# Optimization experiments

Measured on AMD Instinct MI355X. Metric: run time of the kernel, lower is better.

The kernel has to match this reference:

```python
import jax, jax.numpy as jnp
import numpy as np

B, C, H, W = 4, 128, 100, 256
M = 2

def setup_inputs() -> dict:
    key = jax.random.key(0)
    ks = jax.random.split(key, 5)
    feat0 = jax.random.normal(ks[0], (B, C, H, W), jnp.float32)
    feat1 = jax.random.normal(ks[1], (B, C, H, W), jnp.float32)
    adapter_weight = jax.random.normal(ks[2], (M, C), jnp.float32)
    # conv: 1x1 Conv2d(M*C -> C); store as [C_out, C_in]
    conv_w = jax.random.normal(ks[3], (C, M * C), jnp.float32) * (1.0 / np.sqrt(M * C))
    conv_b = jnp.zeros((C,), jnp.float32)
    mlp_w = jax.random.normal(ks[4], (C, C), jnp.float32) * (1.0 / np.sqrt(C))
    mlp_b = jnp.zeros((C,), jnp.float32)
    return {"feat0": feat0, "feat1": feat1, "adapter_weight": adapter_weight,
            "conv_w": conv_w, "conv_b": conv_b, "mlp_w": mlp_w, "mlp_b": mlp_b}

def reference(feat0, feat1, adapter_weight, conv_w, conv_b, mlp_w, mlp_b):
    feats = jnp.stack([feat0, feat1], axis=0)              # [M, B, C, H, W]
    b, c, h, w = feat0.shape
    # per-modality scalar-per-channel scale, then concat on channel dim
    scaled = feats * adapter_weight[:, None, :, None, None]
    cat = scaled.transpose(1, 0, 2, 3, 4).reshape(b, -1, h, w)  # [B, M*C, H, W]
    # 1x1 conv == channel matmul
    fused = jnp.einsum('bkhw,ck->bchw', cat, conv_w) + conv_b[None, :, None, None]
    f = fused.transpose(2, 3, 0, 1).reshape(h * w, b, c)   # [(HW), B, C]
    fm = feats.transpose(0, 3, 4, 1, 2).reshape(len(feats), h * w, b, c)  # [M, (HW), B, C]
    # per-location cross-agent attention, summed over modalities
    scores = jnp.einsum('msbc,sdc->msbd', fm, f) / np.sqrt(c).astype(jnp.float32)
    attn = jax.nn.softmax(scores, axis=-1)                 # [M, (HW), B, B]
    retrieved = jnp.einsum('msbd,sdc->sbc', attn, f)       # summed over m
    out = f + jax.nn.relu(retrieved @ mlp_w.T + mlp_b)
    return out.reshape(h, w, b, c).transpose(2, 3, 0, 1)   # [B, C, H, W]
```

## Files before the change

kernel.cpp:

```cpp
#include <hip/hip_runtime.h>

#define HW 25600
#define TS 16
#define NT 1600
#define NB 256

typedef float  f32x4   __attribute__((ext_vector_type(4)));
typedef short  short8  __attribute__((ext_vector_type(8)));
typedef short  short4v __attribute__((ext_vector_type(4)));
typedef unsigned int uint2v __attribute__((ext_vector_type(2)));
typedef unsigned int uint4v __attribute__((ext_vector_type(4)));

__device__ __forceinline__ float bf2f(short h) {
    return __builtin_bit_cast(float, (unsigned)((unsigned short)h) << 16);
}
__device__ __forceinline__ unsigned cvt_pk(float a, float b) {
    unsigned r;
    asm("v_cvt_pk_bf16_f32 %0, %1, %2" : "=v"(r) : "v"(a), "v"(b));
    return r;
}

typedef __attribute__((address_space(3))) const char lds_cchar;
typedef __attribute__((address_space(3))) char lds_char;
typedef __attribute__((address_space(1))) const void g_cvoid;
__device__ __forceinline__ unsigned lds_u32(const void* p) {
    return (unsigned)(uintptr_t)(lds_cchar*)p;
}
__device__ __forceinline__ void dma16(const float* g, unsigned lds_byte) {
    __builtin_amdgcn_global_load_lds(
        (g_cvoid*)g,
        (__attribute__((address_space(3))) void*)(lds_char*)(uintptr_t)lds_byte,
        16, 0, 0);
}

__device__ __forceinline__ short4v tr_read(unsigned a) {
    short4v d;
    asm volatile("ds_read_b64_tr_b16 %0, %1" : "=v"(d) : "v"(a) : "memory");
    return d;
}
__device__ __forceinline__ short4v tr_read128(unsigned a) {
    short4v d;
    asm volatile("ds_read_b64_tr_b16 %0, %1 offset:128" : "=v"(d) : "v"(a) : "memory");
    return d;
}
__device__ __forceinline__ uint4v lds_b128(unsigned a) {
    uint4v d;
    asm volatile("ds_read_b128 %0, %1" : "=v"(d) : "v"(a) : "memory");
    return d;
}
__device__ __forceinline__ void wait_lgkm8() {
    asm volatile("s_waitcnt lgkmcnt(8)" ::: "memory");
    __builtin_amdgcn_sched_barrier(0);
}
__device__ __forceinline__ void wait_lgkm6() {
    asm volatile("s_waitcnt lgkmcnt(6)" ::: "memory");
    __builtin_amdgcn_sched_barrier(0);
}
__device__ __forceinline__ void wait_lgkm0() {
    asm volatile("s_waitcnt lgkmcnt(0)" ::: "memory");
    __builtin_amdgcn_sched_barrier(0);
}
__device__ __forceinline__ void wait_vm0() {
    asm volatile("s_waitcnt vmcnt(0)" ::: "memory");
    __builtin_amdgcn_sched_barrier(0);
}
__device__ __forceinline__ void bar_lgkm() {
    asm volatile("s_waitcnt lgkmcnt(0)" ::: "memory");
    __builtin_amdgcn_s_barrier();
    asm volatile("" ::: "memory");
}

struct Clu { short4v lo0, hi0, lo1, hi1, lo2, hi2, lo3, hi3; };
__device__ __forceinline__ void issue_clu(Clu& C, unsigned base, int tstride) {
    C.lo0 = tr_read(base);                C.hi0 = tr_read128(base);
    C.lo1 = tr_read(base + tstride);      C.hi1 = tr_read128(base + tstride);
    C.lo2 = tr_read(base + 2 * tstride);  C.hi2 = tr_read128(base + 2 * tstride);
    C.lo3 = tr_read(base + 3 * tstride);  C.hi3 = tr_read128(base + 3 * tstride);
}
__device__ __forceinline__ short8 mk8(short4v lo, short4v hi) {
    return __builtin_shufflevector(lo, hi, 0, 1, 2, 3, 4, 5, 6, 7);
}

__global__ __launch_bounds__(512, 2) void mmf_kernel(
    const float* __restrict__ feat0, const float* __restrict__ feat1,
    const float* __restrict__ adapter, const float* __restrict__ conv_w,
    const float* __restrict__ conv_b, const float* __restrict__ mlp_w,
    const float* __restrict__ mlp_b, float* __restrict__ out)
{
    __shared__ __align__(128) char smem[133120];
    float* Xf32 = (float*)smem;
    short* Xbf  = (short*)(smem + 65536);
    short* fbf  = (short*)(smem + 98304);
    short* Rbf  = (short*)(smem + 114688);
    float* sc   = (float*)(smem + 131072);

    const int tid = threadIdx.x;
    const int bid = blockIdx.x;
    const int xcd  = bid & 7;
    const int jb   = bid >> 3;
    const int tbeg = 200 * xcd + jb;
    const int tend = 200 * (xcd + 1);
    const int w   = __builtin_amdgcn_readfirstlane(tid >> 6);
    const int l   = tid & 63;
    const int g   = l >> 4;
    const int sl  = l & 15;
    const int c0  = w * 16;

    const unsigned xfbase = lds_u32(Xf32);
    const unsigned xbase  = lds_u32(Xbf);

    auto stage_dma = [&](int S) {
        #pragma unroll
        for (int i = 0; i < 8; ++i) {
            int idx = i * 512 + tid;
            int q  = idx & 3;
            int r  = idx >> 2;
            int cc = r & 127;
            int b  = (r >> 7) & 3;
            int m  = r >> 9;
            const float* fp = m ? feat1 : feat0;
            dma16(fp + (size_t)((b * 128 + cc) * HW + S + q * 4),
                  xfbase + (unsigned)((i * 512 + (w << 6)) << 4));
        }
    };

    stage_dma(tbeg * TS);

    short8 afc[8];
    #pragma unroll
    for (int ks = 0; ks < 8; ++ks) {
        const int k0 = ks * 32 + g * 8;
        const float4 w0 = *reinterpret_cast<const float4*>(conv_w + (c0 + sl) * 256 + k0);
        const float4 w1 = *reinterpret_cast<const float4*>(conv_w + (c0 + sl) * 256 + k0 + 4);
        const float4 a0 = *reinterpret_cast<const float4*>(adapter + k0);
        const float4 a1 = *reinterpret_cast<const float4*>(adapter + k0 + 4);
        uint4v au;
        au[0] = cvt_pk(w0.x * a0.x, w0.y * a0.y);
        au[1] = cvt_pk(w0.z * a0.z, w0.w * a0.w);
        au[2] = cvt_pk(w1.x * a1.x, w1.y * a1.y);
        au[3] = cvt_pk(w1.z * a1.z, w1.w * a1.w);
        afc[ks] = __builtin_bit_cast(short8, au);
    }
    short8 afm[4];
    #pragma unroll
    for (int ks = 0; ks < 4; ++ks) {
        const int k0 = ks * 32 + g * 8;
        const float4 w0 = *reinterpret_cast<const float4*>(mlp_w + (c0 + sl) * 128 + k0);
        const float4 w1 = *reinterpret_cast<const float4*>(mlp_w + (c0 + sl) * 128 + k0 + 4);
        uint4v au;
        au[0] = cvt_pk(w0.x, w0.y);
        au[1] = cvt_pk(w0.z, w0.w);
        au[2] = cvt_pk(w1.x, w1.y);
        au[3] = cvt_pk(w1.z, w1.w);
        afm[ks] = __builtin_bit_cast(short8, au);
    }
    float bias[4], mb[4];
    #pragma unroll
    for (int i = 0; i < 4; ++i) {
        bias[i] = conv_b[c0 + g * 4 + i];
        mb[i]   = mlp_b[c0 + g * 4 + i];
    }
    wait_vm0();
    bar_lgkm();

    for (int ti = tbeg; ti < tend; ti += 32) {
        const int S = ti * TS;

        #pragma unroll
        for (int i = 0; i < 8; ++i) {
            int idx = i * 512 + tid;
            const float4 v = *reinterpret_cast<const float4*>(Xf32 + (size_t)idx * 4);
            int q  = idx & 3;
            int r  = idx >> 2;
            int cc = r & 127;
            int b  = (r >> 7) & 3;
            int m  = r >> 9;
            uint2v xv;
            xv[0] = cvt_pk(v.x, v.y);
            xv[1] = cvt_pk(v.z, v.w);
            *reinterpret_cast<uint2v*>(Xbf + b * 4096 + (m * 128 + cc) * 16 + q * 4) = xv;
        }
        bar_lgkm();

        if (ti + 32 < tend) stage_dma((ti + 32) * TS);

        {
            f32x4 acc[4] = {{0,0,0,0},{0,0,0,0},{0,0,0,0},{0,0,0,0}};
            Clu cA, cB;
            issue_clu(cA, xbase + 0 * 1024 + g * 256 + sl * 8, 8192);
            #pragma unroll
            for (int ks = 0; ks < 8; ++ks) {
                Clu& cur = (ks & 1) ? cB : cA;
                Clu& nxt = (ks & 1) ? cA : cB;
                if (ks < 7) {
                    issue_clu(nxt, xbase + (ks + 1) * 1024 + g * 256 + sl * 8, 8192);
                    wait_lgkm8();
                } else {
                    wait_lgkm0();
                }
                acc[0] = __builtin_amdgcn_mfma_f32_16x16x32_bf16(afc[ks], mk8(cur.lo0, cur.hi0), acc[0], 0, 0, 0);
                acc[1] = __builtin_amdgcn_mfma_f32_16x16x32_bf16(afc[ks], mk8(cur.lo1, cur.hi1), acc[1], 0, 0, 0);
                acc[2] = __builtin_amdgcn_mfma_f32_16x16x32_bf16(afc[ks], mk8(cur.lo2, cur.hi2), acc[2], 0, 0, 0);
                acc[3] = __builtin_amdgcn_mfma_f32_16x16x32_bf16(afc[ks], mk8(cur.lo3, cur.hi3), acc[3], 0, 0, 0);
            }
            #pragma unroll
            for (int tt = 0; tt < 4; ++tt) {
                const int col = tt * 16 + sl;
                uint2v fu;
                fu[0] = cvt_pk(acc[tt][0] + bias[0], acc[tt][1] + bias[1]);
                fu[1] = cvt_pk(acc[tt][2] + bias[2], acc[tt][3] + bias[3]);
                *reinterpret_cast<uint2v*>(fbf + col * 128 + (((c0 + g * 4) ^ (sl << 3)) ^ (tt << 5))) = fu;
            }
        }
        bar_lgkm();

        {
            const int sm_m = w >> 2;
            const int sm_b = w & 3;
            const int ad = sl >> 2;
            const int aq = sl & 3;
            const unsigned fbase = lds_u32(fbf);
            const unsigned btile = xbase + sm_b * 8192 + sm_m * 4096 + g * 256 + sl * 8;
            f32x4 accS[4] = {{0,0,0,0},{0,0,0,0},{0,0,0,0},{0,0,0,0}};
            struct SC { short4v blo, bhi; uint4v a0, a1, a2, a3; };
            SC pA, pB;
            auto issue = [&](SC& Sv, int kk) {
                const unsigned bt = btile + (unsigned)(kk * 1024);
                Sv.blo = tr_read(bt); Sv.bhi = tr_read128(bt);
                const int cg = kk * 4 + g;
                Sv.a0 = lds_b128(fbase + (unsigned)((ad * 16 + 0 + aq) * 256 + (((cg ^ (0 + aq)) ^ (ad << 2)) << 4)));
                Sv.a1 = lds_b128(fbase + (unsigned)((ad * 16 + 4 + aq) * 256 + (((cg ^ (4 + aq)) ^ (ad << 2)) << 4)));
                Sv.a2 = lds_b128(fbase + (unsigned)((ad * 16 + 8 + aq) * 256 + (((cg ^ (8 + aq)) ^ (ad << 2)) << 4)));
                Sv.a3 = lds_b128(fbase + (unsigned)((ad * 16 + 12 + aq) * 256 + (((cg ^ (12 + aq)) ^ (ad << 2)) << 4)));
            };
            issue(pA, 0);
            #pragma unroll
            for (int kk = 0; kk < 4; ++kk) {
                SC& cur = (kk & 1) ? pB : pA;
                SC& nxt = (kk & 1) ? pA : pB;
                if (kk < 3) {
                    issue(nxt, kk + 1);
                    wait_lgkm6();
                } else {
                    wait_lgkm0();
                }
                const short8 bf = mk8(cur.blo, cur.bhi);
                accS[0] = __builtin_amdgcn_mfma_f32_16x16x32_bf16(__builtin_bit_cast(short8, cur.a0), bf, accS[0], 0, 0, 0);
                accS[1] = __builtin_amdgcn_mfma_f32_16x16x32_bf16(__builtin_bit_cast(short8, cur.a1), bf, accS[1], 0, 0, 0);
                accS[2] = __builtin_amdgcn_mfma_f32_16x16x32_bf16(__builtin_bit_cast(short8, cur.a2), bf, accS[2], 0, 0, 0);
                accS[3] = __builtin_amdgcn_mfma_f32_16x16x32_bf16(__builtin_bit_cast(short8, cur.a3), bf, accS[3], 0, 0, 0);
            }
            const int cstar = sl >> 2, qstar = sl & 3;
            float x = accS[0][0];
            #pragma unroll
            for (int c = 0; c < 4; ++c)
                #pragma unroll
                for (int q = 0; q < 4; ++q)
                    if (c == cstar && q == qstar) x = accS[c][q];
            x *= 0.088388347648318447f;
            float mx = fmaxf(x, __shfl_xor(x, 16));
            mx = fmaxf(mx, __shfl_xor(mx, 32));
            float e = __expf(x - mx);
            float sm = e + __shfl_xor(e, 16);
            sm += __shfl_xor(sm, 32);
            sc[(sm_m * 16 + sm_b * 4 + g) * 16 + sl] = e / sm;
        }
        bar_lgkm();

        {
            const int b = l >> 4, s = l & 15;
            float aw[4];
            #pragma unroll
            for (int d = 0; d < 4; ++d)
                aw[d] = sc[(b * 4 + d) * 16 + s] + sc[(16 + b * 4 + d) * 16 + s];
            #pragma unroll
            for (int h = 0; h < 2; ++h) {
                const int cb = w * 2 + h;
                float r[8] = {0,0,0,0,0,0,0,0};
                #pragma unroll
                for (int d = 0; d < 4; ++d) {
                    const int colf = d * 16 + s;
                    short8 fv = *reinterpret_cast<const short8*>(
                        fbf + colf * 128 + (((cb ^ s) ^ (d << 2)) << 3));
                    #pragma unroll
                    for (int e = 0; e < 8; ++e) r[e] += aw[d] * bf2f(fv[e]);
                }
                #pragma unroll
                for (int e = 0; e < 8; e += 2) {
                    unsigned uu = cvt_pk(r[e], r[e + 1]);
                    Rbf[b * 2048 + (cb * 8 + e) * 16 + s]     = (short)(uu & 0xffffu);
                    Rbf[b * 2048 + (cb * 8 + e + 1) * 16 + s] = (short)(uu >> 16);
                }
            }
        }
        bar_lgkm();

        {
            f32x4 acc[4] = {{0,0,0,0},{0,0,0,0},{0,0,0,0},{0,0,0,0}};
            const unsigned rbase = lds_u32(Rbf);
            Clu cA, cB;
            issue_clu(cA, rbase + 0 * 1024 + g * 256 + sl * 8, 4096);
            #pragma unroll
            for (int ks = 0; ks < 4; ++ks) {
                Clu& cur = (ks & 1) ? cB : cA;
                Clu& nxt = (ks & 1) ? cA : cB;
                if (ks < 3) {
                    issue_clu(nxt, rbase + (ks + 1) * 1024 + g * 256 + sl * 8, 4096);
                    wait_lgkm8();
                } else {
                    wait_lgkm0();
                }
                acc[0] = __builtin_amdgcn_mfma_f32_16x16x32_bf16(afm[ks], mk8(cur.lo0, cur.hi0), acc[0], 0, 0, 0);
                acc[1] = __builtin_amdgcn_mfma_f32_16x16x32_bf16(afm[ks], mk8(cur.lo1, cur.hi1), acc[1], 0, 0, 0);
                acc[2] = __builtin_amdgcn_mfma_f32_16x16x32_bf16(afm[ks], mk8(cur.lo2, cur.hi2), acc[2], 0, 0, 0);
                acc[3] = __builtin_amdgcn_mfma_f32_16x16x32_bf16(afm[ks], mk8(cur.lo3, cur.hi3), acc[3], 0, 0, 0);
            }
            wait_vm0();
            #pragma unroll
            for (int tt = 0; tt < 4; ++tt) {
                const int col = tt * 16 + sl;
                const short4v res = *reinterpret_cast<const short4v*>(
                    fbf + col * 128 + (((c0 + g * 4) ^ (sl << 3)) ^ (tt << 5)));
                #pragma unroll
                for (int i = 0; i < 4; ++i) {
                    const int c = c0 + g * 4 + i;
                    float v = fmaxf(acc[tt][i] + mb[i], 0.f) + bf2f(res[i]);
                    out[(size_t)(tt * 128 + c) * HW + S + sl] = v;
                }
            }
        }
        bar_lgkm();
    }
}

extern "C" void kernel_launch(void* const* d_in, const int* in_sizes, int n_in,
                              void* d_out, int out_size, void* d_ws, size_t ws_size,
                              hipStream_t stream) {
    const float* feat0   = (const float*)d_in[0];
    const float* feat1   = (const float*)d_in[1];
    const float* adapter = (const float*)d_in[2];
    const float* conv_w  = (const float*)d_in[3];
    const float* conv_b  = (const float*)d_in[4];
    const float* mlp_w   = (const float*)d_in[5];
    const float* mlp_b   = (const float*)d_in[6];
    float* out = (float*)d_out;

    dim3 grid(NB);
    dim3 block(512);
    hipLaunchKernelGGL(mmf_kernel, grid, block, 0, stream,
                       feat0, feat1, adapter, conv_w, conv_b, mlp_w, mlp_b, out);
}
```

Baseline: 49.09 us.

## Tile both GEMMs as 2x2 channel-by-batch blocks per wave to halve LDS B-fragment reads

Each wave now computes a 32-channel by 2-batch tile instead of 16 channels by all 4 batches, for both the conv GEMM and the MLP GEMM. Each B fragment read from LDS is reused across two A fragments, so per-wave transposed LDS reads drop by half, and the wait count is lowered to match the smaller prefetch. In exchange each wave holds twice as many weight fragments in registers (afc2/afm2), which raises VGPR pressure and could hurt occupancy under the 512x2 launch bounds.

After: 67.28 us. 1.37x slower.

```diff
diff --git a/kernel.cpp b/kernel.cpp
--- a/kernel.cpp
+++ b/kernel.cpp
@@ -48,8 +48,8 @@
     asm volatile("ds_read_b128 %0, %1" : "=v"(d) : "v"(a) : "memory");
     return d;
 }
-__device__ __forceinline__ void wait_lgkm8() {
-    asm volatile("s_waitcnt lgkmcnt(8)" ::: "memory");
+__device__ __forceinline__ void wait_lgkm4() {
+    asm volatile("s_waitcnt lgkmcnt(4)" ::: "memory");
     __builtin_amdgcn_sched_barrier(0);
 }
 __device__ __forceinline__ void wait_lgkm6() {
@@ -70,12 +70,10 @@
     asm volatile("" ::: "memory");
 }
 
-struct Clu { short4v lo0, hi0, lo1, hi1, lo2, hi2, lo3, hi3; };
-__device__ __forceinline__ void issue_clu(Clu& C, unsigned base, int tstride) {
+struct Clu2 { short4v lo0, hi0, lo1, hi1; };
+__device__ __forceinline__ void issue_clu2(Clu2& C, unsigned base, int tstride) {
     C.lo0 = tr_read(base);                C.hi0 = tr_read128(base);
     C.lo1 = tr_read(base + tstride);      C.hi1 = tr_read128(base + tstride);
-    C.lo2 = tr_read(base + 2 * tstride);  C.hi2 = tr_read128(base + 2 * tstride);
-    C.lo3 = tr_read(base + 3 * tstride);  C.hi3 = tr_read128(base + 3 * tstride);
 }
 __device__ __forceinline__ short8 mk8(short4v lo, short4v hi) {
     return __builtin_shufflevector(lo, hi, 0, 1, 2, 3, 4, 5, 6, 7);
@@ -104,7 +102,8 @@
     const int l   = tid & 63;
     const int g   = l >> 4;
     const int sl  = l & 15;
-    const int c0  = w * 16;
+    const int wc  = w >> 1;
+    const int wb  = w & 1;
 
     const unsigned xfbase = lds_u32(Xf32);
     const unsigned xbase  = lds_u32(Xbf);
@@ -126,40 +125,50 @@
 
     stage_dma(tbeg * TS);
 
-    short8 afc[8];
+    short8 afc2[2][8];
     #pragma unroll
-    for (int ks = 0; ks < 8; ++ks) {
-        const int k0 = ks * 32 + g * 8;
-        const float4 w0 = *reinterpret_cast<const float4*>(conv_w + (c0 + sl) * 256 + k0);
-        const float4 w1 = *reinterpret_cast<const float4*>(conv_w + (c0 + sl) * 256 + k0 + 4);
-        const float4 a0 = *reinterpret_cast<const float4*>(adapter + k0);
-        const float4 a1 = *reinterpret_cast<const float4*>(adapter + k0 + 4);
-        uint4v au;
-        au[0] = cvt_pk(w0.x * a0.x, w0.y * a0.y);
-        au[1] = cvt_pk(w0.z * a0.z, w0.w * a0.w);
-        au[2] = cvt_pk(w1.x * a1.x, w1.y * a1.y);
-        au[3] = cvt_pk(w1.z * a1.z, w1.w * a1.w);
-        afc[ks] = __builtin_bit_cast(short8, au);
+    for (int cc2 = 0; cc2 < 2; ++cc2) {
+        const int crow = wc * 32 + cc2 * 16 + sl;
+        #pragma unroll
+        for (int ks = 0; ks < 8; ++ks) {
+            const int k0 = ks * 32 + g * 8;
+            const float4 w0 = *reinterpret_cast<const float4*>(conv_w + crow * 256 + k0);
+            const float4 w1 = *reinterpret_cast<const float4*>(conv_w + crow * 256 + k0 + 4);
+            const float4 a0 = *reinterpret_cast<const float4*>(adapter + k0);
+            const float4 a1 = *reinterpret_cast<const float4*>(adapter + k0 + 4);
+            uint4v au;
+            au[0] = cvt_pk(w0.x * a0.x, w0.y * a0.y);
+            au[1] = cvt_pk(w0.z * a0.z, w0.w * a0.w);
+            au[2] = cvt_pk(w1.x * a1.x, w1.y * a1.y);
+            au[3] = cvt_pk(w1.z * a1.z, w1.w * a1.w);
+            afc2[cc2][ks] = __builtin_bit_cast(short8, au);
+        }
     }
-    short8 afm[4];
+    short8 afm2[2][4];
     #pragma unroll
-    for (int ks = 0; ks < 4; ++ks) {
-        const int k0 = ks * 32 + g * 8;
-        const float4 w0 = *reinterpret_cast<const float4*>(mlp_w + (c0 + sl) * 128 + k0);
-        const float4 w1 = *reinterpret_cast<const float4*>(mlp_w + (c0 + sl) * 128 + k0 + 4);
-        uint4v au;
-        au[0] = cvt_pk(w0.x, w0.y);
-        au[1] = cvt_pk(w0.z, w0.w);
-        au[2] = cvt_pk(w1.x, w1.y);
-        au[3] = cvt_pk(w1.z, w1.w);
-        afm[ks] = __builtin_bit_cast(short8, au);
+    for (int cc2 = 0; cc2 < 2; ++cc2) {
+        const int crow = wc * 32 + cc2 * 16 + sl;
+        #pragma unroll
+        for (int ks = 0; ks < 4; ++ks) {
+            const int k0 = ks * 32 + g * 8;
+            const float4 w0 = *reinterpret_cast<const float4*>(mlp_w + crow * 128 + k0);
+            const float4 w1 = *reinterpret_cast<const float4*>(mlp_w + crow * 128 + k0 + 4);
+            uint4v au;
+            au[0] = cvt_pk(w0.x, w0.y);
+            au[1] = cvt_pk(w0.z, w0.w);
+            au[2] = cvt_pk(w1.x, w1.y);
+            au[3] = cvt_pk(w1.z, w1.w);
+            afm2[cc2][ks] = __builtin_bit_cast(short8, au);
+        }
     }
-    float bias[4], mb[4];
+    float bias2[2][4], mb2[2][4];
     #pragma unroll
-    for (int i = 0; i < 4; ++i) {
-        bias[i] = conv_b[c0 + g * 4 + i];
-        mb[i]   = mlp_b[c0 + g * 4 + i];
-    }
+    for (int cc2 = 0; cc2 < 2; ++cc2)
+        #pragma unroll
+        for (int i = 0; i < 4; ++i) {
+            bias2[cc2][i] = conv_b[wc * 32 + cc2 * 16 + g * 4 + i];
+            mb2[cc2][i]   = mlp_b[wc * 32 + cc2 * 16 + g * 4 + i];
+        }
     wait_vm0();
     bar_lgkm();
 
@@ -185,31 +194,41 @@
         if (ti + 32 < tend) stage_dma((ti + 32) * TS);
 
         {
-            f32x4 acc[4] = {{0,0,0,0},{0,0,0,0},{0,0,0,0},{0,0,0,0}};
-            Clu cA, cB;
-            issue_clu(cA, xbase + 0 * 1024 + g * 256 + sl * 8, 8192);
+            f32x4 a00 = {0,0,0,0}, a01 = {0,0,0,0};
+            f32x4 a10 = {0,0,0,0}, a11 = {0,0,0,0};
+            const unsigned cb0 = xbase + (unsigned)(wb * 16384) + g * 256 + sl * 8;
+            Clu2 cA, cB;
+            issue_clu2(cA, cb0, 8192);
             #pragma unroll
             for (int ks = 0; ks < 8; ++ks) {
-                Clu& cur = (ks & 1) ? cB : cA;
-                Clu& nxt = (ks & 1) ? cA : cB;
+                Clu2& cur = (ks & 1) ? cB : cA;
+                Clu2& nxt = (ks & 1) ? cA : cB;
                 if (ks < 7) {
-                    issue_clu(nxt, xbase + (ks + 1) * 1024 + g * 256 + sl * 8, 8192);
-                    wait_lgkm8();
+                    issue_clu2(nxt, cb0 + (unsigned)((ks + 1) * 1024), 8192);
+                    wait_lgkm4();
                 } else {
                     wait_lgkm0();
                 }
-                acc[0] = __builtin_amdgcn_mfma_f32_16x16x32_bf16(afc[ks], mk8(cur.lo0, cur.hi0), acc[0], 0, 0, 0);
-                acc[1] = __builtin_amdgcn_mfma_f32_16x16x32_bf16(afc[ks], mk8(cur.lo1, cur.hi1), acc[1], 0, 0, 0);
-                acc[2] = __builtin_amdgcn_mfma_f32_16x16x32_bf16(afc[ks], mk8(cur.lo2, cur.hi2), acc[2], 0, 0, 0);
-                acc[3] = __builtin_amdgcn_mfma_f32_16x16x32_bf16(afc[ks], mk8(cur.lo3, cur.hi3), acc[3], 0, 0, 0);
-            }
-            #pragma unroll
-            for (int tt = 0; tt < 4; ++tt) {
-                const int col = tt * 16 + sl;
-                uint2v fu;
-                fu[0] = cvt_pk(acc[tt][0] + bias[0], acc[tt][1] + bias[1]);
-                fu[1] = cvt_pk(acc[tt][2] + bias[2], acc[tt][3] + bias[3]);
-                *reinterpret_cast<uint2v*>(fbf + col * 128 + (((c0 + g * 4) ^ (sl << 3)) ^ (tt << 5))) = fu;
+                const short8 b0 = mk8(cur.lo0, cur.hi0);
+                const short8 b1 = mk8(cur.lo1, cur.hi1);
+                a00 = __builtin_amdgcn_mfma_f32_16x16x32_bf16(afc2[0][ks], b0, a00, 0, 0, 0);
+                a01 = __builtin_amdgcn_mfma_f32_16x16x32_bf16(afc2[0][ks], b1, a01, 0, 0, 0);
+                a10 = __builtin_amdgcn_mfma_f32_16x16x32_bf16(afc2[1][ks], b0, a10, 0, 0, 0);
+                a11 = __builtin_amdgcn_mfma_f32_16x16x32_bf16(afc2[1][ks], b1, a11, 0, 0, 0);
+            }
+            #pragma unroll
+            for (int cc2 = 0; cc2 < 2; ++cc2) {
+                const int cX = wc * 32 + cc2 * 16 + g * 4;
+                #pragma unroll
+                for (int bb = 0; bb < 2; ++bb) {
+                    const f32x4& ac = cc2 ? (bb ? a11 : a10) : (bb ? a01 : a00);
+                    const int b   = wb * 2 + bb;
+                    const int col = b * 16 + sl;
+                    uint2v fu;
+                    fu[0] = cvt_pk(ac[0] + bias2[cc2][0], ac[1] + bias2[cc2][1]);
+                    fu[1] = cvt_pk(ac[2] + bias2[cc2][2], ac[3] + bias2[cc2][3]);
+                    *reinterpret_cast<uint2v*>(fbf + col * 128 + ((cX ^ (sl << 3)) ^ (b << 5))) = fu;
+                }
             }
         }
         bar_lgkm();
@@ -296,36 +315,46 @@
         bar_lgkm();
 
         {
-            f32x4 acc[4] = {{0,0,0,0},{0,0,0,0},{0,0,0,0},{0,0,0,0}};
+            f32x4 a00 = {0,0,0,0}, a01 = {0,0,0,0};
+            f32x4 a10 = {0,0,0,0}, a11 = {0,0,0,0};
             const unsigned rbase = lds_u32(Rbf);
-            Clu cA, cB;
-            issue_clu(cA, rbase + 0 * 1024 + g * 256 + sl * 8, 4096);
+            const unsigned rb0 = rbase + (unsigned)(wb * 8192) + g * 256 + sl * 8;
+            Clu2 cA, cB;
+            issue_clu2(cA, rb0, 4096);
             #pragma unroll
             for (int ks = 0; ks < 4; ++ks) {
-                Clu& cur = (ks & 1) ? cB : cA;
-                Clu& nxt = (ks & 1) ? cA : cB;
+                Clu2& cur = (ks & 1) ? cB : cA;
+                Clu2& nxt = (ks & 1) ? cA : cB;
                 if (ks < 3) {
-                    issue_clu(nxt, rbase + (ks + 1) * 1024 + g * 256 + sl * 8, 4096);
-                    wait_lgkm8();
+                    issue_clu2(nxt, rb0 + (unsigned)((ks + 1) * 1024), 4096);
+                    wait_lgkm4();
                 } else {
                     wait_lgkm0();
                 }
-                acc[0] = __builtin_amdgcn_mfma_f32_16x16x32_bf16(afm[ks], mk8(cur.lo0, cur.hi0), acc[0], 0, 0, 0);
-                acc[1] = __builtin_amdgcn_mfma_f32_16x16x32_bf16(afm[ks], mk8(cur.lo1, cur.hi1), acc[1], 0, 0, 0);
-                acc[2] = __builtin_amdgcn_mfma_f32_16x16x32_bf16(afm[ks], mk8(cur.lo2, cur.hi2), acc[2], 0, 0, 0);
-                acc[3] = __builtin_amdgcn_mfma_f32_16x16x32_bf16(afm[ks], mk8(cur.lo3, cur.hi3), acc[3], 0, 0, 0);
+                const short8 b0 = mk8(cur.lo0, cur.hi0);
+                const short8 b1 = mk8(cur.lo1, cur.hi1);
+                a00 = __builtin_amdgcn_mfma_f32_16x16x32_bf16(afm2[0][ks], b0, a00, 0, 0, 0);
+                a01 = __builtin_amdgcn_mfma_f32_16x16x32_bf16(afm2[0][ks], b1, a01, 0, 0, 0);
+                a10 = __builtin_amdgcn_mfma_f32_16x16x32_bf16(afm2[1][ks], b0, a10, 0, 0, 0);
+                a11 = __builtin_amdgcn_mfma_f32_16x16x32_bf16(afm2[1][ks], b1, a11, 0, 0, 0);
             }
             wait_vm0();
             #pragma unroll
-            for (int tt = 0; tt < 4; ++tt) {
-                const int col = tt * 16 + sl;
-                const short4v res = *reinterpret_cast<const short4v*>(
-                    fbf + col * 128 + (((c0 + g * 4) ^ (sl << 3)) ^ (tt << 5)));
-                #pragma unroll
-                for (int i = 0; i < 4; ++i) {
-                    const int c = c0 + g * 4 + i;
-                    float v = fmaxf(acc[tt][i] + mb[i], 0.f) + bf2f(res[i]);
-                    out[(size_t)(tt * 128 + c) * HW + S + sl] = v;
+            for (int cc2 = 0; cc2 < 2; ++cc2) {
+                const int cX = wc * 32 + cc2 * 16 + g * 4;
+                #pragma unroll
+                for (int bb = 0; bb < 2; ++bb) {
+                    const f32x4& ac = cc2 ? (bb ? a11 : a10) : (bb ? a01 : a00);
+                    const int b   = wb * 2 + bb;
+                    const int col = b * 16 + sl;
+                    const short4v res = *reinterpret_cast<const short4v*>(
+                        fbf + col * 128 + ((cX ^ (sl << 3)) ^ (b << 5)));
+                    #pragma unroll
+                    for (int i = 0; i < 4; ++i) {
+                        const int c = cX + i;
+                        float v = fmaxf(ac[i] + mb2[cc2][i], 0.f) + bf2f(res[i]);
+                        out[(size_t)(b * 128 + c) * HW + S + sl] = v;
+                    }
                 }
             }
         }
```
